# Kernel tuning notes

Measured on AMD Instinct MI355X. Metric: run time of the kernel, lower is better.

Reference implementation:

```python
import jax, jax.numpy as jnp
import numpy as np

TOP_K = 512  # int(node_num * K) = int(2048 * 0.25)
NEG = -1.0e12
SLOPE = 0.01  # nn.LeakyReLU default negative_slope


def setup_inputs() -> dict:
    key = jax.random.key(0)
    k1, k2, k3, k4 = jax.random.split(key, 4)
    B, N, in_c, out_c, gs = 8, 2048, 128, 128, 128
    x = jax.random.normal(k1, (B, N, in_c), dtype=jnp.float32)
    W = jax.random.normal(k2, (in_c, out_c), dtype=jnp.float32) * (1.0 / np.sqrt(in_c))
    a = jax.random.normal(k3, (2 * out_c, 1), dtype=jnp.float32) * (1.0 / np.sqrt(2 * out_c))
    GL = jax.random.normal(k4, (N, gs), dtype=jnp.float32) * (1.0 / np.sqrt(gs))
    return {"x": x, "W": W, "a": a, "GL": GL}


def reference(x, W, a, GL):
    B, N, _ = x.shape
    out_c = W.shape[1]
    # learned adjacency: softmax(relu(GL GL^T)) + I  -> [N, N]
    adj = jax.nn.softmax(jax.nn.relu(GL @ GL.T), axis=-1) + jnp.eye(N, dtype=GL.dtype)
    h = x @ W  # [B, N, out_c]
    # e[b,i,j] = LeakyReLU( [h_i ; h_j] . a ) = LeakyReLU( h_i.a1 + h_j.a2 )
    # (avoids materializing the [B, N*N, 2*out_c] concat of the original)
    a1, a2 = a[:out_c, 0], a[out_c:, 0]
    e = jax.nn.leaky_relu((h @ a1)[:, :, None] + (h @ a2)[:, None, :], SLOPE)  # [B,N,N]
    att = jnp.where(adj[None] > 0, e, NEG)
    # top-k along dim=1 (rows, per column j): transpose so that axis is last
    att_t = jnp.swapaxes(att, 1, 2)  # [B, Nj, Ni]
    _, idx = jax.lax.top_k(att_t, TOP_K)  # idx: [B, Nj, TOP_K]
    b_ix = jnp.arange(B)[:, None, None]
    j_ix = jnp.arange(N)[None, :, None]
    mask_t = jnp.zeros_like(att_t).at[b_ix, j_ix, idx].set(1.0)
    mask = jnp.swapaxes(mask_t, 1, 2)  # [B, Ni, Nj]
    att = jax.nn.softmax(att * mask, axis=2)
    h_prime = jax.nn.relu(att @ h)  # [B, N, out_c]
    return jnp.swapaxes(h_prime, -2, -1)  # [B, out_c, N]
```

## Files before the change

### kernel.cpp

```cpp
#include <hip/hip_runtime.h>
#include <math.h>


#define B_ 8
#define N_ 2048
#define C_ 128
#define TOPK_ 512
#define NCH_ 32
#define CL_ 64
#define NP1_ 2052
#define RANKB_ 256

#define H_OFF    ((size_t)0)
#define P_OFF    (H_OFF + (size_t)B_*N_*C_)
#define Q_OFF    (P_OFF + (size_t)B_*N_)
#define LOK_OFF  (Q_OFF + (size_t)B_*N_)
#define US_OFF   (LOK_OFF + (size_t)B_*N_)
#define VS_OFF   (US_OFF + (size_t)B_*N_)
#define SRT_OFF  (VS_OFF + (size_t)B_*N_)
#define SUS_OFF  (SRT_OFF + (size_t)B_*N_)
#define PVS_OFF  (SUS_OFF + (size_t)B_*NP1_)
#define SUL_OFF  (PVS_OFF + (size_t)B_*NP1_)
#define PVL_OFF  (SUL_OFF + (size_t)B_*N_*128)
#define TOTU_OFF (PVL_OFF + (size_t)B_*N_*128)
#define TOTV_OFF (TOTU_OFF + (size_t)B_*NCH_*128)
#define MPART_OFF (TOTV_OFF + (size_t)B_*NCH_*128)

__global__ __launch_bounds__(256) void k_pq(const float* __restrict__ x,
                                            const float* __restrict__ W,
                                            const float* __restrict__ a,
                                            float* __restrict__ p,
                                            float* __restrict__ q) {
  __shared__ float al[256];
  __shared__ float wa1[128], wa2[128];
  const int t = threadIdx.x;
  const int r0 = blockIdx.x * 64;
  al[t] = a[t];
  __syncthreads();
  if (t < 128) {
    const float* Wr = W + (size_t)t * 128;
    float s1 = 0.f, s2 = 0.f;
#pragma unroll
    for (int j = 0; j < 128; j += 4) {
      float4 wv = *(const float4*)(Wr + j);
      s1 = fmaf(wv.x, al[j + 0], s1);
      s1 = fmaf(wv.y, al[j + 1], s1);
      s1 = fmaf(wv.z, al[j + 2], s1);
      s1 = fmaf(wv.w, al[j + 3], s1);
      s2 = fmaf(wv.x, al[128 + j + 0], s2);
      s2 = fmaf(wv.y, al[128 + j + 1], s2);
      s2 = fmaf(wv.z, al[128 + j + 2], s2);
      s2 = fmaf(wv.w, al[128 + j + 3], s2);
    }
    wa1[t] = s1; wa2[t] = s2;
  }
  __syncthreads();
  const int row = t >> 2, part = t & 3;
  const float* xr = x + (size_t)(r0 + row) * 128 + part * 32;
  const float* w1 = wa1 + part * 32;
  const float* w2 = wa2 + part * 32;
  float sp = 0.f, sq = 0.f;
#pragma unroll
  for (int i = 0; i < 8; ++i) {
    float4 xv = *(const float4*)(xr + 4 * i);
    float4 w1v = *(const float4*)(w1 + 4 * i);
    float4 w2v = *(const float4*)(w2 + 4 * i);
    sp = fmaf(xv.x, w1v.x, sp); sp = fmaf(xv.y, w1v.y, sp);
    sp = fmaf(xv.z, w1v.z, sp); sp = fmaf(xv.w, w1v.w, sp);
    sq = fmaf(xv.x, w2v.x, sq); sq = fmaf(xv.y, w2v.y, sq);
    sq = fmaf(xv.z, w2v.z, sq); sq = fmaf(xv.w, w2v.w, sq);
  }
  sp += __shfl_xor(sp, 1, 64); sp += __shfl_xor(sp, 2, 64);
  sq += __shfl_xor(sq, 1, 64); sq += __shfl_xor(sq, 2, 64);
  if (part == 0) { p[r0 + row] = sp; q[r0 + row] = sq; }
}

__global__ __launch_bounds__(512, 4) void k_fuse(
    const float* __restrict__ x, const float* __restrict__ W,
    float* __restrict__ h, float* __restrict__ mpart,
    const float* __restrict__ q, const float* __restrict__ p,
    float* __restrict__ u_s, float* __restrict__ v_s,
    int* __restrict__ srt, int* __restrict__ lok) {
  union __align__(16) SMem {
    struct { float Wl[64 * 128]; float xl[64 * 68]; } g;
    struct { float ql[N_]; float pl[N_]; } r;
  };
  __shared__ SMem sm;
  const int blk = blockIdx.x, t = threadIdx.x;

  if (blk < RANKB_) {
    const int b = blk >> 5, tile = blk & 31;
    const int i0 = tile * 64;
    ((float4*)sm.r.ql)[t] = ((const float4*)(q + (size_t)b * N_))[t];
    ((float4*)sm.r.pl)[t] = ((const float4*)(p + (size_t)b * N_))[t];
    __syncthreads();
    const int row = t >> 3, s = t & 7;
    const int i = i0 + row;
    const float qi = sm.r.ql[i], pi = sm.r.pl[i];
    const float negpi = -pi;
    int qr = 0, lo = 0, pr = 0;
    for (int g = s; g < 512; g += 8) {
      float4 qj = ((const float4*)sm.r.ql)[g];
      float4 pj = ((const float4*)sm.r.pl)[g];
      const int j0 = 4 * g;
      qr += (qj.x < qi || (qj.x == qi && (j0 + 0) < i)) ? 1 : 0;
      qr += (qj.y < qi || (qj.y == qi && (j0 + 1) < i)) ? 1 : 0;
      qr += (qj.z < qi || (qj.z == qi && (j0 + 2) < i)) ? 1 : 0;
      qr += (qj.w < qi || (qj.w == qi && (j0 + 3) < i)) ? 1 : 0;
      lo += (qj.x < negpi) ? 1 : 0;
      lo += (qj.y < negpi) ? 1 : 0;
      lo += (qj.z < negpi) ? 1 : 0;
      lo += (qj.w < negpi) ? 1 : 0;
      pr += (pj.x > pi || (pj.x == pi && (j0 + 0) < i)) ? 1 : 0;
      pr += (pj.y > pi || (pj.y == pi && (j0 + 1) < i)) ? 1 : 0;
      pr += (pj.z > pi || (pj.z == pi && (j0 + 2) < i)) ? 1 : 0;
      pr += (pj.w > pi || (pj.w == pi && (j0 + 3) < i)) ? 1 : 0;
    }
    qr += __shfl_xor(qr, 1, 64); qr += __shfl_xor(qr, 2, 64); qr += __shfl_xor(qr, 4, 64);
    lo += __shfl_xor(lo, 1, 64); lo += __shfl_xor(lo, 2, 64); lo += __shfl_xor(lo, 4, 64);
    pr += __shfl_xor(pr, 1, 64); pr += __shfl_xor(pr, 2, 64); pr += __shfl_xor(pr, 4, 64);
    if (s == 0) {
      u_s[(size_t)b * N_ + qr] = __expf(qi);
      v_s[(size_t)b * N_ + qr] = __expf(0.01f * qi);
      srt[(size_t)b * N_ + qr] = i;
      lok[(size_t)b * N_ + i] = lo | ((pr < TOPK_) ? 0x10000 : 0);
    }
    return;
  }

  float* Wl = sm.g.Wl;
  float* xl = sm.g.xl;
  const int g = blk - RANKB_;
  const int r0 = g * 64;
  const int cg = t & 15, rp = (t >> 4) & 15;
  const bool act = t < 256;
  float acc[4][8];
#pragma unroll
  for (int r = 0; r < 4; ++r)
#pragma unroll
    for (int j = 0; j < 8; ++j) acc[r][j] = 0.f;

  for (int kc = 0; kc < 2; ++kc) {
    __syncthreads();
    const float4* W4 = (const float4*)(W + (size_t)kc * 64 * 128);
    float4* Wl4 = (float4*)Wl;
#pragma unroll
    for (int i = 0; i < 4; ++i) Wl4[t + 512 * i] = W4[t + 512 * i];
#pragma unroll
    for (int i = 0; i < 2; ++i) {
      int idx = t + 512 * i;
      int row = idx >> 4, c4i = idx & 15;
      float4 v = *(const float4*)(x + (size_t)(r0 + row) * 128 + kc * 64 + c4i * 4);
      ((float4*)xl)[row * 17 + c4i] = v;
    }
    __syncthreads();
    if (act) {
      for (int k = 0; k < 64; ++k) {
        const float4* Wr = (const float4*)(Wl + k * 128);
        float4 w0 = Wr[cg];
        float4 w1 = Wr[cg + 16];
#pragma unroll
        for (int r = 0; r < 4; ++r) {
          float xv = xl[(4 * rp + r) * 68 + k];
          acc[r][0] = fmaf(xv, w0.x, acc[r][0]);
          acc[r][1] = fmaf(xv, w0.y, acc[r][1]);
          acc[r][2] = fmaf(xv, w0.z, acc[r][2]);
          acc[r][3] = fmaf(xv, w0.w, acc[r][3]);
          acc[r][4] = fmaf(xv, w1.x, acc[r][4]);
          acc[r][5] = fmaf(xv, w1.y, acc[r][5]);
          acc[r][6] = fmaf(xv, w1.z, acc[r][6]);
          acc[r][7] = fmaf(xv, w1.w, acc[r][7]);
        }
      }
    }
  }
  const int c0 = 4 * cg, c1 = 4 * cg + 64;
  size_t hb = (size_t)r0 * 128;
  __syncthreads();
  float* scratch = xl;
  if (act) {
#pragma unroll
    for (int r = 0; r < 4; ++r) {
      int row = 4 * rp + r;
      *(float4*)(h + hb + (size_t)row * 128 + c0) =
          make_float4(acc[r][0], acc[r][1], acc[r][2], acc[r][3]);
      *(float4*)(h + hb + (size_t)row * 128 + c1) =
          make_float4(acc[r][4], acc[r][5], acc[r][6], acc[r][7]);
    }
#pragma unroll
    for (int j = 0; j < 4; ++j) {
      scratch[rp * 128 + c0 + j] = acc[0][j] + acc[1][j] + acc[2][j] + acc[3][j];
      scratch[rp * 128 + c1 + j] = acc[0][4 + j] + acc[1][4 + j] + acc[2][4 + j] + acc[3][4 + j];
    }
  }
  __syncthreads();
  if (t < 128) {
    float s = 0.f;
#pragma unroll
    for (int rr = 0; rr < 16; ++rr) s += scratch[rr * 128 + t];
    mpart[(size_t)g * 128 + t] = s;
  }
}

__global__ __launch_bounds__(256) void k_scan(const float* __restrict__ h,
                                              const float* __restrict__ u_s,
                                              const float* __restrict__ v_s,
                                              const int* __restrict__ srt,
                                              float* __restrict__ SUl,
                                              float* __restrict__ PVl,
                                              float* __restrict__ totU,
                                              float* __restrict__ totV,
                                              float* __restrict__ SUS,
                                              float* __restrict__ PVS) {
  __shared__ float hl[CL_][128];
  __shared__ float ul[CL_], vl[CL_];
  __shared__ int sl[CL_];
  __shared__ float2 sa[256], sb[256];
  const int t = threadIdx.x;
  if (blockIdx.x >= 256) {
    const int b = blockIdx.x - 256;
    float4 ua = ((const float4*)(u_s + (size_t)b * N_))[2 * t];
    float4 ub = ((const float4*)(u_s + (size_t)b * N_))[2 * t + 1];
    float4 wa = ((const float4*)(v_s + (size_t)b * N_))[2 * t];
    float4 wb = ((const float4*)(v_s + (size_t)b * N_))[2 * t + 1];
    float su = ua.x + ua.y + ua.z + ua.w + ub.x + ub.y + ub.z + ub.w;
    float sw = wa.x + wa.y + wa.z + wa.w + wb.x + wb.y + wb.z + wb.w;
    sa[t] = make_float2(su, sw);
    __syncthreads();
    float2* cur = sa; float2* nxt = sb;
    for (int off = 1; off < 256; off <<= 1) {
      float2 vv = cur[t];
      if (t >= off) { float2 o = cur[t - off]; vv.x += o.x; vv.y += o.y; }
      nxt[t] = vv;
      __syncthreads();
      float2* tmp = cur; cur = nxt; nxt = tmp;
    }
    float2 incl = cur[t];
    float2 tot = cur[255];
    float exclU = incl.x - su, exclW = incl.y - sw;
    float s0 = tot.x - exclU;
    float s1 = s0 - ua.x, s2 = s1 - ua.y, s3 = s2 - ua.z;
    float s4 = s3 - ua.w, s5 = s4 - ub.x, s6 = s5 - ub.y, s7 = s6 - ub.z;
    float p0 = exclW;
    float p1 = p0 + wa.x, p2 = p1 + wa.y, p3 = p2 + wa.z;
    float p4 = p3 + wa.w, p5 = p4 + wb.x, p6 = p5 + wb.y, p7 = p6 + wb.z;
    float* Sb = SUS + (size_t)b * NP1_ + 8 * t;
    float* Pb = PVS + (size_t)b * NP1_ + 8 * t;
    *(float4*)(Sb) = make_float4(s0, s1, s2, s3);
    *(float4*)(Sb + 4) = make_float4(s4, s5, s6, s7);
    *(float4*)(Pb) = make_float4(p0, p1, p2, p3);
    *(float4*)(Pb + 4) = make_float4(p4, p5, p6, p7);
    if (t == 255) {
      SUS[(size_t)b * NP1_ + N_] = 0.f;
      PVS[(size_t)b * NP1_ + N_] = tot.y;
    }
    return;
  }
  const int b = blockIdx.x >> 5, ch = blockIdx.x & 31;
  const int base = b * N_ + ch * CL_;
  if (t < CL_) { ul[t] = u_s[base + t]; vl[t] = v_s[base + t]; sl[t] = srt[base + t]; }
  __syncthreads();
  {
    const int c4 = t & 31, rr = t >> 5;
#pragma unroll
    for (int i = 0; i < 8; ++i) {
      int tt = rr + 8 * i;
      float4 v = *(const float4*)(h + ((size_t)b * N_ + sl[tt]) * 128 + 4 * c4);
      *(float4*)(&hl[tt][4 * c4]) = v;
    }
  }
  __syncthreads();
  if (t < 128) {
    const int c = t;
    float run = 0.f;
    for (int tt = CL_ - 1; tt >= 0; --tt) {
      run = fmaf(ul[tt], hl[tt][c], run);
      SUl[((size_t)(base + tt)) * 128 + c] = run;
    }
    totU[(size_t)(b * NCH_ + ch) * 128 + c] = run;
  } else {
    const int c = t - 128;
    float run2 = 0.f;
    for (int tt = 0; tt < CL_; ++tt) {
      PVl[((size_t)(base + tt)) * 128 + c] = run2;
      run2 = fmaf(vl[tt], hl[tt][c], run2);
    }
    totV[(size_t)(b * NCH_ + ch) * 128 + c] = run2;
  }
}

__global__ __launch_bounds__(256) void k_out(const float* __restrict__ p,
                                             const int* __restrict__ lok,
                                             const float* __restrict__ SUS,
                                             const float* __restrict__ PVS,
                                             const float* __restrict__ SUl,
                                             const float* __restrict__ PVl,
                                             const float* __restrict__ totU,
                                             const float* __restrict__ totV,
                                             const float* __restrict__ mpart,
                                             float* __restrict__ out) {
  __shared__ float res[64 * 129];
  __shared__ float CSUs[(NCH_ + 1) * 128];
  __shared__ float CPVs[(NCH_ + 1) * 128];
  __shared__ float mr[128];
  __shared__ float A_s[64], B_s[64], invD[64];
  __shared__ int lo_s[64], keep_s[64];
  const int b = blockIdx.x >> 5, tile = blockIdx.x & 31;
  const int t = threadIdx.x;
  const int i0 = tile * 64;
  if (t < 128) {
    float ms = 0.f;
#pragma unroll
    for (int j = 0; j < 32; ++j) ms += mpart[(size_t)(b * 32 + j) * 128 + t];
    mr[t] = fmaxf(ms * (1.0f / (float)N_), 0.f);
    float s = 0.f;
    CSUs[NCH_ * 128 + t] = 0.f;
    for (int cc = NCH_ - 1; cc >= 0; --cc) {
      s += totU[(size_t)(b * NCH_ + cc) * 128 + t];
      CSUs[cc * 128 + t] = s;
    }
  } else {
    const int c2 = t - 128;
    float s2 = 0.f;
    for (int cc = 0; cc < NCH_; ++cc) {
      CPVs[cc * 128 + c2] = s2;
      s2 += totV[(size_t)(b * NCH_ + cc) * 128 + c2];
    }
    CPVs[NCH_ * 128 + c2] = s2;
  }
  __syncthreads();
  if (t < 64) {
    float pv = p[b * N_ + i0 + t];
    int lk = lok[(size_t)b * N_ + i0 + t];
    keep_s[t] = (lk >> 16) & 1;
    int lo = lk & 0xFFFF;
    lo_s[t] = lo;
    float A = __expf(pv), Bv = __expf(0.01f * pv);
    A_s[t] = A; B_s[t] = Bv;
    float sus = SUS[(size_t)b * NP1_ + lo];
    float pvs = PVS[(size_t)b * NP1_ + lo];
    invD[t] = 1.0f / fmaf(A, sus, Bv * pvs);
  }
  __syncthreads();
  const int half = t >> 7, c = t & 127;
#pragma unroll 4
  for (int ii2 = 0; ii2 < 64; ii2 += 2) {
    int ii = ii2 + half;
    float outv;
    if (keep_s[ii]) {
      int lo = lo_s[ii];
      float A = A_s[ii], Bv = B_s[ii];
      float suc, pvc;
      if (lo < N_) {
        int chn = lo >> 6;
        size_t ro = ((size_t)(b * N_ + lo)) * 128;
        suc = SUl[ro + c] + CSUs[(chn + 1) * 128 + c];
        pvc = PVl[ro + c] + CPVs[chn * 128 + c];
      } else {
        suc = 0.f;
        pvc = CPVs[NCH_ * 128 + c];
      }
      outv = fmaxf(fmaf(A, suc, Bv * pvc) * invD[ii], 0.f);
    } else {
      outv = mr[c];
    }
    res[ii * 129 + c] = outv;
  }
  __syncthreads();
#pragma unroll
  for (int pass = 0; pass < 8; ++pass) {
    int cc = (t >> 4) + pass * 16;
    int ii4 = (t & 15) * 4;
    float4 v;
    v.x = res[(ii4 + 0) * 129 + cc];
    v.y = res[(ii4 + 1) * 129 + cc];
    v.z = res[(ii4 + 2) * 129 + cc];
    v.w = res[(ii4 + 3) * 129 + cc];
    *(float4*)(out + ((size_t)(b * C_ + cc)) * N_ + i0 + ii4) = v;
  }
}

extern "C" void kernel_launch(void* const* d_in, const int* in_sizes, int n_in,
                              void* d_out, int out_size, void* d_ws, size_t ws_size,
                              hipStream_t stream) {
  (void)in_sizes; (void)n_in; (void)out_size; (void)ws_size;
  const float* x = (const float*)d_in[0];
  const float* W = (const float*)d_in[1];
  const float* a = (const float*)d_in[2];
  float* out = (float*)d_out;
  float* ws = (float*)d_ws;

  float* h    = ws + H_OFF;
  float* p    = ws + P_OFF;
  float* q    = ws + Q_OFF;
  int*   lok  = (int*)(ws + LOK_OFF);
  float* u_s  = ws + US_OFF;
  float* v_s  = ws + VS_OFF;
  int*   srt  = (int*)(ws + SRT_OFF);
  float* SUS  = ws + SUS_OFF;
  float* PVS  = ws + PVS_OFF;
  float* SUl  = ws + SUL_OFF;
  float* PVl  = ws + PVL_OFF;
  float* totU = ws + TOTU_OFF;
  float* totV = ws + TOTV_OFF;
  float* mpart = ws + MPART_OFF;

  k_pq<<<dim3((B_ * N_) / 64), dim3(256), 0, stream>>>(x, W, a, p, q);
  k_fuse<<<dim3(RANKB_ + (B_ * N_) / 64), dim3(512), 0, stream>>>(
      x, W, h, mpart, q, p, u_s, v_s, srt, lok);
  k_scan<<<dim3(256 + B_), dim3(256), 0, stream>>>(h, u_s, v_s, srt, SUl, PVl, totU, totV, SUS, PVS);
  k_out<<<dim3(B_ * 32), dim3(256), 0, stream>>>(p, lok, SUS, PVS, SUl, PVl, totU, totV, mpart, out);
}
```

Measured before the change: 104.3 us.

## Defer W projection: scan over x, apply W after attention aggregation

Uses linearity to run the prefix-scan attention aggregation directly on x rather than on h = xW. The 128x128 W multiply is then done once per output tile inside k_out, and the relu of the mean is applied after projecting the mean of x. This drops the separate h GEMM kernel and its write and read of h, folding the column mean of x into k_pq. The ranking work moves to its own k_rank kernel. k_out now takes on a 64x128x128 GEMM and loads a 64KB W tile into shared memory, which raises LDS use and may lower occupancy.

```diff
diff --git a/kernel.cpp b/kernel.cpp
--- a/kernel.cpp
+++ b/kernel.cpp
@@ -9,10 +9,8 @@
 #define NCH_ 32
 #define CL_ 64
 #define NP1_ 2052
-#define RANKB_ 256
-
-#define H_OFF    ((size_t)0)
-#define P_OFF    (H_OFF + (size_t)B_*N_*C_)
+
+#define P_OFF    ((size_t)0)
 #define Q_OFF    (P_OFF + (size_t)B_*N_)
 #define LOK_OFF  (Q_OFF + (size_t)B_*N_)
 #define US_OFF   (LOK_OFF + (size_t)B_*N_)
@@ -20,19 +18,21 @@
 #define SRT_OFF  (VS_OFF + (size_t)B_*N_)
 #define SUS_OFF  (SRT_OFF + (size_t)B_*N_)
 #define PVS_OFF  (SUS_OFF + (size_t)B_*NP1_)
-#define SUL_OFF  (PVS_OFF + (size_t)B_*NP1_)
-#define PVL_OFF  (SUL_OFF + (size_t)B_*N_*128)
-#define TOTU_OFF (PVL_OFF + (size_t)B_*N_*128)
+#define SUX_OFF  (PVS_OFF + (size_t)B_*NP1_)
+#define PVX_OFF  (SUX_OFF + (size_t)B_*N_*128)
+#define TOTU_OFF (PVX_OFF + (size_t)B_*N_*128)
 #define TOTV_OFF (TOTU_OFF + (size_t)B_*NCH_*128)
-#define MPART_OFF (TOTV_OFF + (size_t)B_*NCH_*128)
+#define XPART_OFF (TOTV_OFF + (size_t)B_*NCH_*128)
 
 __global__ __launch_bounds__(256) void k_pq(const float* __restrict__ x,
                                             const float* __restrict__ W,
                                             const float* __restrict__ a,
                                             float* __restrict__ p,
-                                            float* __restrict__ q) {
+                                            float* __restrict__ q,
+                                            float* __restrict__ xpart) {
   __shared__ float al[256];
   __shared__ float wa1[128], wa2[128];
+  __shared__ float xps[2][128];
   const int t = threadIdx.x;
   const int r0 = blockIdx.x * 64;
   al[t] = a[t];
@@ -55,159 +55,93 @@
     wa1[t] = s1; wa2[t] = s2;
   }
   __syncthreads();
-  const int row = t >> 2, part = t & 3;
-  const float* xr = x + (size_t)(r0 + row) * 128 + part * 32;
-  const float* w1 = wa1 + part * 32;
-  const float* w2 = wa2 + part * 32;
-  float sp = 0.f, sq = 0.f;
-#pragma unroll
-  for (int i = 0; i < 8; ++i) {
-    float4 xv = *(const float4*)(xr + 4 * i);
-    float4 w1v = *(const float4*)(w1 + 4 * i);
-    float4 w2v = *(const float4*)(w2 + 4 * i);
-    sp = fmaf(xv.x, w1v.x, sp); sp = fmaf(xv.y, w1v.y, sp);
-    sp = fmaf(xv.z, w1v.z, sp); sp = fmaf(xv.w, w1v.w, sp);
-    sq = fmaf(xv.x, w2v.x, sq); sq = fmaf(xv.y, w2v.y, sq);
-    sq = fmaf(xv.z, w2v.z, sq); sq = fmaf(xv.w, w2v.w, sq);
-  }
-  sp += __shfl_xor(sp, 1, 64); sp += __shfl_xor(sp, 2, 64);
-  sq += __shfl_xor(sq, 1, 64); sq += __shfl_xor(sq, 2, 64);
-  if (part == 0) { p[r0 + row] = sp; q[r0 + row] = sq; }
-}
-
-__global__ __launch_bounds__(512, 4) void k_fuse(
-    const float* __restrict__ x, const float* __restrict__ W,
-    float* __restrict__ h, float* __restrict__ mpart,
-    const float* __restrict__ q, const float* __restrict__ p,
-    float* __restrict__ u_s, float* __restrict__ v_s,
-    int* __restrict__ srt, int* __restrict__ lok) {
-  union __align__(16) SMem {
-    struct { float Wl[64 * 128]; float xl[64 * 68]; } g;
-    struct { float ql[N_]; float pl[N_]; } r;
-  };
-  __shared__ SMem sm;
+  {
+    const int row = t >> 2, part = t & 3;
+    const float* xr = x + (size_t)(r0 + row) * 128 + part * 32;
+    const float* w1 = wa1 + part * 32;
+    const float* w2 = wa2 + part * 32;
+    float sp = 0.f, sq = 0.f;
+#pragma unroll
+    for (int i = 0; i < 8; ++i) {
+      float4 xv = *(const float4*)(xr + 4 * i);
+      float4 w1v = *(const float4*)(w1 + 4 * i);
+      float4 w2v = *(const float4*)(w2 + 4 * i);
+      sp = fmaf(xv.x, w1v.x, sp); sp = fmaf(xv.y, w1v.y, sp);
+      sp = fmaf(xv.z, w1v.z, sp); sp = fmaf(xv.w, w1v.w, sp);
+      sq = fmaf(xv.x, w2v.x, sq); sq = fmaf(xv.y, w2v.y, sq);
+      sq = fmaf(xv.z, w2v.z, sq); sq = fmaf(xv.w, w2v.w, sq);
+    }
+    sp += __shfl_xor(sp, 1, 64); sp += __shfl_xor(sp, 2, 64);
+    sq += __shfl_xor(sq, 1, 64); sq += __shfl_xor(sq, 2, 64);
+    if (part == 0) { p[r0 + row] = sp; q[r0 + row] = sq; }
+  }
+  {
+    const int cc = t & 127, hh = t >> 7;
+    float s = 0.f;
+    for (int r2 = 32 * hh; r2 < 32 * hh + 32; ++r2)
+      s += x[(size_t)(r0 + r2) * 128 + cc];
+    xps[hh][cc] = s;
+  }
+  __syncthreads();
+  if (t < 128)
+    xpart[(size_t)blockIdx.x * 128 + t] = xps[0][t] + xps[1][t];
+}
+
+__global__ __launch_bounds__(256) void k_rank(const float* __restrict__ q,
+                                              const float* __restrict__ p,
+                                              float* __restrict__ u_s,
+                                              float* __restrict__ v_s,
+                                              int* __restrict__ srt,
+                                              int* __restrict__ lok) {
+  __shared__ float ql[N_], pl[N_];
   const int blk = blockIdx.x, t = threadIdx.x;
-
-  if (blk < RANKB_) {
-    const int b = blk >> 5, tile = blk & 31;
-    const int i0 = tile * 64;
-    ((float4*)sm.r.ql)[t] = ((const float4*)(q + (size_t)b * N_))[t];
-    ((float4*)sm.r.pl)[t] = ((const float4*)(p + (size_t)b * N_))[t];
-    __syncthreads();
-    const int row = t >> 3, s = t & 7;
-    const int i = i0 + row;
-    const float qi = sm.r.ql[i], pi = sm.r.pl[i];
-    const float negpi = -pi;
-    int qr = 0, lo = 0, pr = 0;
-    for (int g = s; g < 512; g += 8) {
-      float4 qj = ((const float4*)sm.r.ql)[g];
-      float4 pj = ((const float4*)sm.r.pl)[g];
-      const int j0 = 4 * g;
-      qr += (qj.x < qi || (qj.x == qi && (j0 + 0) < i)) ? 1 : 0;
-      qr += (qj.y < qi || (qj.y == qi && (j0 + 1) < i)) ? 1 : 0;
-      qr += (qj.z < qi || (qj.z == qi && (j0 + 2) < i)) ? 1 : 0;
-      qr += (qj.w < qi || (qj.w == qi && (j0 + 3) < i)) ? 1 : 0;
-      lo += (qj.x < negpi) ? 1 : 0;
-      lo += (qj.y < negpi) ? 1 : 0;
-      lo += (qj.z < negpi) ? 1 : 0;
-      lo += (qj.w < negpi) ? 1 : 0;
-      pr += (pj.x > pi || (pj.x == pi && (j0 + 0) < i)) ? 1 : 0;
-      pr += (pj.y > pi || (pj.y == pi && (j0 + 1) < i)) ? 1 : 0;
-      pr += (pj.z > pi || (pj.z == pi && (j0 + 2) < i)) ? 1 : 0;
-      pr += (pj.w > pi || (pj.w == pi && (j0 + 3) < i)) ? 1 : 0;
-    }
-    qr += __shfl_xor(qr, 1, 64); qr += __shfl_xor(qr, 2, 64); qr += __shfl_xor(qr, 4, 64);
-    lo += __shfl_xor(lo, 1, 64); lo += __shfl_xor(lo, 2, 64); lo += __shfl_xor(lo, 4, 64);
-    pr += __shfl_xor(pr, 1, 64); pr += __shfl_xor(pr, 2, 64); pr += __shfl_xor(pr, 4, 64);
-    if (s == 0) {
-      u_s[(size_t)b * N_ + qr] = __expf(qi);
-      v_s[(size_t)b * N_ + qr] = __expf(0.01f * qi);
-      srt[(size_t)b * N_ + qr] = i;
-      lok[(size_t)b * N_ + i] = lo | ((pr < TOPK_) ? 0x10000 : 0);
-    }
-    return;
-  }
-
-  float* Wl = sm.g.Wl;
-  float* xl = sm.g.xl;
-  const int g = blk - RANKB_;
-  const int r0 = g * 64;
-  const int cg = t & 15, rp = (t >> 4) & 15;
-  const bool act = t < 256;
-  float acc[4][8];
-#pragma unroll
-  for (int r = 0; r < 4; ++r)
-#pragma unroll
-    for (int j = 0; j < 8; ++j) acc[r][j] = 0.f;
-
-  for (int kc = 0; kc < 2; ++kc) {
-    __syncthreads();
-    const float4* W4 = (const float4*)(W + (size_t)kc * 64 * 128);
-    float4* Wl4 = (float4*)Wl;
-#pragma unroll
-    for (int i = 0; i < 4; ++i) Wl4[t + 512 * i] = W4[t + 512 * i];
-#pragma unroll
-    for (int i = 0; i < 2; ++i) {
-      int idx = t + 512 * i;
-      int row = idx >> 4, c4i = idx & 15;
-      float4 v = *(const float4*)(x + (size_t)(r0 + row) * 128 + kc * 64 + c4i * 4);
-      ((float4*)xl)[row * 17 + c4i] = v;
-    }
-    __syncthreads();
-    if (act) {
-      for (int k = 0; k < 64; ++k) {
-        const float4* Wr = (const float4*)(Wl + k * 128);
-        float4 w0 = Wr[cg];
-        float4 w1 = Wr[cg + 16];
-#pragma unroll
-        for (int r = 0; r < 4; ++r) {
-          float xv = xl[(4 * rp + r) * 68 + k];
-          acc[r][0] = fmaf(xv, w0.x, acc[r][0]);
-          acc[r][1] = fmaf(xv, w0.y, acc[r][1]);
-          acc[r][2] = fmaf(xv, w0.z, acc[r][2]);
-          acc[r][3] = fmaf(xv, w0.w, acc[r][3]);
-          acc[r][4] = fmaf(xv, w1.x, acc[r][4]);
-          acc[r][5] = fmaf(xv, w1.y, acc[r][5]);
-          acc[r][6] = fmaf(xv, w1.z, acc[r][6]);
-          acc[r][7] = fmaf(xv, w1.w, acc[r][7]);
-        }
-      }
-    }
-  }
-  const int c0 = 4 * cg, c1 = 4 * cg + 64;
-  size_t hb = (size_t)r0 * 128;
-  __syncthreads();
-  float* scratch = xl;
-  if (act) {
-#pragma unroll
-    for (int r = 0; r < 4; ++r) {
-      int row = 4 * rp + r;
-      *(float4*)(h + hb + (size_t)row * 128 + c0) =
-          make_float4(acc[r][0], acc[r][1], acc[r][2], acc[r][3]);
-      *(float4*)(h + hb + (size_t)row * 128 + c1) =
-          make_float4(acc[r][4], acc[r][5], acc[r][6], acc[r][7]);
-    }
-#pragma unroll
-    for (int j = 0; j < 4; ++j) {
-      scratch[rp * 128 + c0 + j] = acc[0][j] + acc[1][j] + acc[2][j] + acc[3][j];
-      scratch[rp * 128 + c1 + j] = acc[0][4 + j] + acc[1][4 + j] + acc[2][4 + j] + acc[3][4 + j];
-    }
-  }
-  __syncthreads();
-  if (t < 128) {
-    float s = 0.f;
-#pragma unroll
-    for (int rr = 0; rr < 16; ++rr) s += scratch[rr * 128 + t];
-    mpart[(size_t)g * 128 + t] = s;
-  }
-}
-
-__global__ __launch_bounds__(256) void k_scan(const float* __restrict__ h,
+  const int b = blk >> 5, tile = blk & 31;
+  const int i0 = tile * 64;
+#pragma unroll
+  for (int i = 0; i < 2; ++i) {
+    ((float4*)ql)[t + 256 * i] = ((const float4*)(q + (size_t)b * N_))[t + 256 * i];
+    ((float4*)pl)[t + 256 * i] = ((const float4*)(p + (size_t)b * N_))[t + 256 * i];
+  }
+  __syncthreads();
+  const int row = t >> 2, s = t & 3;
+  const int i = i0 + row;
+  const float qi = ql[i], pi = pl[i];
+  const float negpi = -pi;
+  int qr = 0, lo = 0, pr = 0;
+  for (int g = s; g < 512; g += 4) {
+    float4 qj = ((const float4*)ql)[g];
+    float4 pj = ((const float4*)pl)[g];
+    const int j0 = 4 * g;
+    qr += (qj.x < qi || (qj.x == qi && (j0 + 0) < i)) ? 1 : 0;
+    qr += (qj.y < qi || (qj.y == qi && (j0 + 1) < i)) ? 1 : 0;
+    qr += (qj.z < qi || (qj.z == qi && (j0 + 2) < i)) ? 1 : 0;
+    qr += (qj.w < qi || (qj.w == qi && (j0 + 3) < i)) ? 1 : 0;
+    lo += (qj.x < negpi) ? 1 : 0;
+    lo += (qj.y < negpi) ? 1 : 0;
+    lo += (qj.z < negpi) ? 1 : 0;
+    lo += (qj.w < negpi) ? 1 : 0;
+    pr += (pj.x > pi || (pj.x == pi && (j0 + 0) < i)) ? 1 : 0;
+    pr += (pj.y > pi || (pj.y == pi && (j0 + 1) < i)) ? 1 : 0;
+    pr += (pj.z > pi || (pj.z == pi && (j0 + 2) < i)) ? 1 : 0;
+    pr += (pj.w > pi || (pj.w == pi && (j0 + 3) < i)) ? 1 : 0;
+  }
+  qr += __shfl_xor(qr, 1, 64); qr += __shfl_xor(qr, 2, 64);
+  lo += __shfl_xor(lo, 1, 64); lo += __shfl_xor(lo, 2, 64);
+  pr += __shfl_xor(pr, 1, 64); pr += __shfl_xor(pr, 2, 64);
+  if (s == 0) {
+    u_s[(size_t)b * N_ + qr] = __expf(qi);
+    v_s[(size_t)b * N_ + qr] = __expf(0.01f * qi);
+    srt[(size_t)b * N_ + qr] = i;
+    lok[(size_t)b * N_ + i] = lo | ((pr < TOPK_) ? 0x10000 : 0);
+  }
+}
+
+__global__ __launch_bounds__(256) void k_scan(const float* __restrict__ x,
                                               const float* __restrict__ u_s,
                                               const float* __restrict__ v_s,
                                               const int* __restrict__ srt,
-                                              float* __restrict__ SUl,
-                                              float* __restrict__ PVl,
+                                              float* __restrict__ SUX,
+                                              float* __restrict__ PVX,
                                               float* __restrict__ totU,
                                               float* __restrict__ totV,
                                               float* __restrict__ SUS,
@@ -265,7 +199,7 @@
 #pragma unroll
     for (int i = 0; i < 8; ++i) {
       int tt = rr + 8 * i;
-      float4 v = *(const float4*)(h + ((size_t)b * N_ + sl[tt]) * 128 + 4 * c4);
+      float4 v = *(const float4*)(x + ((size_t)b * N_ + sl[tt]) * 128 + 4 * c4);
       *(float4*)(&hl[tt][4 * c4]) = v;
     }
   }
@@ -275,14 +209,14 @@
     float run = 0.f;
     for (int tt = CL_ - 1; tt >= 0; --tt) {
       run = fmaf(ul[tt], hl[tt][c], run);
-      SUl[((size_t)(base + tt)) * 128 + c] = run;
+      SUX[((size_t)(base + tt)) * 128 + c] = run;
     }
     totU[(size_t)(b * NCH_ + ch) * 128 + c] = run;
   } else {
     const int c = t - 128;
     float run2 = 0.f;
     for (int tt = 0; tt < CL_; ++tt) {
-      PVl[((size_t)(base + tt)) * 128 + c] = run2;
+      PVX[((size_t)(base + tt)) * 128 + c] = run2;
       run2 = fmaf(vl[tt], hl[tt][c], run2);
     }
     totV[(size_t)(b * NCH_ + ch) * 128 + c] = run2;
@@ -293,40 +227,49 @@
                                              const int* __restrict__ lok,
                                              const float* __restrict__ SUS,
                                              const float* __restrict__ PVS,
-                                             const float* __restrict__ SUl,
-                                             const float* __restrict__ PVl,
+                                             const float* __restrict__ SUX,
+                                             const float* __restrict__ PVX,
                                              const float* __restrict__ totU,
                                              const float* __restrict__ totV,
-                                             const float* __restrict__ mpart,
+                                             const float* __restrict__ xpart,
+                                             const float* __restrict__ W,
                                              float* __restrict__ out) {
-  __shared__ float res[64 * 129];
-  __shared__ float CSUs[(NCH_ + 1) * 128];
-  __shared__ float CPVs[(NCH_ + 1) * 128];
-  __shared__ float mr[128];
+  __shared__ float Wl[128 * 128];
+  __shared__ float zl[64 * 132];
+  __shared__ union {
+    struct { float CSU[(NCH_ + 1) * 128]; float CPV[(NCH_ + 1) * 128]; float xm[128]; } tb;
+    float res[64 * 129];
+  } u_;
   __shared__ float A_s[64], B_s[64], invD[64];
   __shared__ int lo_s[64], keep_s[64];
   const int b = blockIdx.x >> 5, tile = blockIdx.x & 31;
   const int t = threadIdx.x;
   const int i0 = tile * 64;
+  {
+    const float4* W4 = (const float4*)W;
+    float4* Wl4 = (float4*)Wl;
+#pragma unroll
+    for (int i = 0; i < 16; ++i) Wl4[t + 256 * i] = W4[t + 256 * i];
+  }
   if (t < 128) {
     float ms = 0.f;
 #pragma unroll
-    for (int j = 0; j < 32; ++j) ms += mpart[(size_t)(b * 32 + j) * 128 + t];
-    mr[t] = fmaxf(ms * (1.0f / (float)N_), 0.f);
+    for (int j = 0; j < 32; ++j) ms += xpart[(size_t)(b * 32 + j) * 128 + t];
+    u_.tb.xm[t] = ms * (1.0f / (float)N_);
     float s = 0.f;
-    CSUs[NCH_ * 128 + t] = 0.f;
+    u_.tb.CSU[NCH_ * 128 + t] = 0.f;
     for (int cc = NCH_ - 1; cc >= 0; --cc) {
       s += totU[(size_t)(b * NCH_ + cc) * 128 + t];
-      CSUs[cc * 128 + t] = s;
+      u_.tb.CSU[cc * 128 + t] = s;
     }
   } else {
     const int c2 = t - 128;
     float s2 = 0.f;
     for (int cc = 0; cc < NCH_; ++cc) {
-      CPVs[cc * 128 + c2] = s2;
+      u_.tb.CPV[cc * 128 + c2] = s2;
       s2 += totV[(size_t)(b * NCH_ + cc) * 128 + c2];
     }
-    CPVs[NCH_ * 128 + c2] = s2;
+    u_.tb.CPV[NCH_ * 128 + c2] = s2;
   }
   __syncthreads();
   if (t < 64) {
@@ -342,29 +285,68 @@
     invD[t] = 1.0f / fmaf(A, sus, Bv * pvs);
   }
   __syncthreads();
-  const int half = t >> 7, c = t & 127;
+  {
+    const int half = t >> 7, c = t & 127;
 #pragma unroll 4
-  for (int ii2 = 0; ii2 < 64; ii2 += 2) {
-    int ii = ii2 + half;
-    float outv;
-    if (keep_s[ii]) {
-      int lo = lo_s[ii];
-      float A = A_s[ii], Bv = B_s[ii];
-      float suc, pvc;
-      if (lo < N_) {
-        int chn = lo >> 6;
-        size_t ro = ((size_t)(b * N_ + lo)) * 128;
-        suc = SUl[ro + c] + CSUs[(chn + 1) * 128 + c];
-        pvc = PVl[ro + c] + CPVs[chn * 128 + c];
+    for (int ii2 = 0; ii2 < 64; ii2 += 2) {
+      int ii = ii2 + half;
+      float zv;
+      if (keep_s[ii]) {
+        int lo = lo_s[ii];
+        float A = A_s[ii], Bv = B_s[ii];
+        float suc, pvc;
+        if (lo < N_) {
+          int chn = lo >> 6;
+          size_t ro = ((size_t)(b * N_ + lo)) * 128;
+          suc = SUX[ro + c] + u_.tb.CSU[(chn + 1) * 128 + c];
+          pvc = PVX[ro + c] + u_.tb.CPV[chn * 128 + c];
+        } else {
+          suc = 0.f;
+          pvc = u_.tb.CPV[NCH_ * 128 + c];
+        }
+        zv = fmaf(A, suc, Bv * pvc) * invD[ii];
       } else {
-        suc = 0.f;
-        pvc = CPVs[NCH_ * 128 + c];
+        zv = u_.tb.xm[c];
       }
-      outv = fmaxf(fmaf(A, suc, Bv * pvc) * invD[ii], 0.f);
-    } else {
-      outv = mr[c];
-    }
-    res[ii * 129 + c] = outv;
+      zl[ii * 132 + c] = zv;
+    }
+  }
+  __syncthreads();
+  const int cg = t & 15, rp = t >> 4;
+  float acc[4][8];
+#pragma unroll
+  for (int r = 0; r < 4; ++r)
+#pragma unroll
+    for (int j = 0; j < 8; ++j) acc[r][j] = 0.f;
+  for (int k = 0; k < 128; ++k) {
+    const float4* Wr = (const float4*)(Wl + k * 128);
+    float4 w0 = Wr[cg];
+    float4 w1 = Wr[cg + 16];
+#pragma unroll
+    for (int r = 0; r < 4; ++r) {
+      float zv = zl[(4 * rp + r) * 132 + k];
+      acc[r][0] = fmaf(zv, w0.x, acc[r][0]);
+      acc[r][1] = fmaf(zv, w0.y, acc[r][1]);
+      acc[r][2] = fmaf(zv, w0.z, acc[r][2]);
+      acc[r][3] = fmaf(zv, w0.w, acc[r][3]);
+      acc[r][4] = fmaf(zv, w1.x, acc[r][4]);
+      acc[r][5] = fmaf(zv, w1.y, acc[r][5]);
+      acc[r][6] = fmaf(zv, w1.z, acc[r][6]);
+      acc[r][7] = fmaf(zv, w1.w, acc[r][7]);
+    }
+  }
+  __syncthreads();
+  {
+    const int c0 = 4 * cg, c1 = 4 * cg + 64;
+#pragma unroll
+    for (int r = 0; r < 4; ++r) {
+      int row = 4 * rp + r;
+#pragma unroll
+      for (int j = 0; j < 4; ++j) {
+        u_.res[row * 129 + c0 + j] = fmaxf(acc[r][j], 0.f);
+        u_.res[row * 129 + c1 + j] = fmaxf(acc[r][4 + j], 0.f);
+      }
+    }
   }
   __syncthreads();
 #pragma unroll
@@ -372,10 +354,10 @@
     int cc = (t >> 4) + pass * 16;
     int ii4 = (t & 15) * 4;
     float4 v;
-    v.x = res[(ii4 + 0) * 129 + cc];
-    v.y = res[(ii4 + 1) * 129 + cc];
-    v.z = res[(ii4 + 2) * 129 + cc];
-    v.w = res[(ii4 + 3) * 129 + cc];
+    v.x = u_.res[(ii4 + 0) * 129 + cc];
+    v.y = u_.res[(ii4 + 1) * 129 + cc];
+    v.z = u_.res[(ii4 + 2) * 129 + cc];
+    v.w = u_.res[(ii4 + 3) * 129 + cc];
     *(float4*)(out + ((size_t)(b * C_ + cc)) * N_ + i0 + ii4) = v;
   }
 }
@@ -390,7 +372,6 @@
   float* out = (float*)d_out;
   float* ws = (float*)d_ws;
 
-  float* h    = ws + H_OFF;
   float* p    = ws + P_OFF;
   float* q    = ws + Q_OFF;
   int*   lok  = (int*)(ws + LOK_OFF);
@@ -399,15 +380,14 @@
   int*   srt  = (int*)(ws + SRT_OFF);
   float* SUS  = ws + SUS_OFF;
   float* PVS  = ws + PVS_OFF;
-  float* SUl  = ws + SUL_OFF;
-  float* PVl  = ws + PVL_OFF;
+  float* SUX  = ws + SUX_OFF;
+  float* PVX  = ws + PVX_OFF;
   float* totU = ws + TOTU_OFF;
   float* totV = ws + TOTV_OFF;
-  float* mpart = ws + MPART_OFF;
-
-  k_pq<<<dim3((B_ * N_) / 64), dim3(256), 0, stream>>>(x, W, a, p, q);
-  k_fuse<<<dim3(RANKB_ + (B_ * N_) / 64), dim3(512), 0, stream>>>(
-      x, W, h, mpart, q, p, u_s, v_s, srt, lok);
-  k_scan<<<dim3(256 + B_), dim3(256), 0, stream>>>(h, u_s, v_s, srt, SUl, PVl, totU, totV, SUS, PVS);
-  k_out<<<dim3(B_ * 32), dim3(256), 0, stream>>>(p, lok, SUS, PVS, SUl, PVl, totU, totV, mpart, out);
-}
+  float* xpart = ws + XPART_OFF;
+
+  k_pq<<<dim3((B_ * N_) / 64), dim3(256), 0, stream>>>(x, W, a, p, q, xpart);
+  k_rank<<<dim3(B_ * 32), dim3(256), 0, stream>>>(q, p, u_s, v_s, srt, lok);
+  k_scan<<<dim3(256 + B_), dim3(256), 0, stream>>>(x, u_s, v_s, srt, SUX, PVX, totU, totV, SUS, PVS);
+  k_out<<<dim3(B_ * 32), dim3(256), 0, stream>>>(p, lok, SUS, PVS, SUX, PVX, totU, totV, xpart, W, out);
+}
```

New measurement: 118.5 us. +13.6%, slower.
